# Performance work log

Measured on AMD Instinct MI355X. Metric: run time of the kernel, lower is better.

The kernel has to match this reference:

```python
import jax, jax.numpy as jnp
import numpy as np

B, S, E, HD = 8, 2048, 1024, 64  # batch, seq, n_embds, head_size (n_embds // n_heads)


def setup_inputs() -> dict:
    key = jax.random.key(0)
    k1, k2, k3, k4 = jax.random.split(key, 4)
    x = jax.random.normal(k1, (B, S, E), dtype=jnp.float32)
    # torch Linear weights have shape [out_features, in_features]; scale like default init
    Wk = jax.random.normal(k2, (HD, E), dtype=jnp.float32) * (1.0 / np.sqrt(E))
    Wq = jax.random.normal(k3, (HD, E), dtype=jnp.float32) * (1.0 / np.sqrt(E))
    Wv = jax.random.normal(k4, (HD, E), dtype=jnp.float32) * (1.0 / np.sqrt(E))
    return {"x": x, "Wk": Wk, "Wq": Wq, "Wv": Wv}


def reference(x, Wk, Wq, Wv):
    # q, k, v: [B, S, HD]
    k = jnp.einsum('bse,he->bsh', x, Wk)
    q = jnp.einsum('bse,he->bsh', x, Wq)
    v = jnp.einsum('bse,he->bsh', x, Wv)
    # scores: [B, S, S], scaled by sqrt(head_size)
    scores = jnp.einsum('bqh,bkh->bqk', q, k) / jnp.sqrt(jnp.float32(HD))
    # causal mask (tril): position q attends to k <= q
    causal = jnp.tril(jnp.ones((S, S), dtype=bool))
    scores = jnp.where(causal, scores, jnp.float32(-jnp.inf))
    attn = jax.nn.softmax(scores, axis=-1)
    # dropout_rate = 0.0 -> identity
    out = jnp.einsum('bqk,bkh->bqh', attn, v)  # [B, S, HD]
    return out
```

## Files before the change

### kernel.cpp

```cpp
#include <hip/hip_runtime.h>
#include <hip/hip_bf16.h>
#include <stdint.h>

typedef short bh8 __attribute__((ext_vector_type(8)));
typedef short bh4 __attribute__((ext_vector_type(4)));
typedef float fx4 __attribute__((ext_vector_type(4)));

#define B_ 8
#define S_ 2048
#define E_ 1024
#define HD_ 64

__device__ __forceinline__ short f2bf(float f) {
  unsigned u = __builtin_bit_cast(unsigned, f);
  u = u + 0x7FFFu + ((u >> 16) & 1u);
  return (short)(u >> 16);
}

#define GL2LDS16(gp, lp) __builtin_amdgcn_global_load_lds( \
    (const __attribute__((address_space(1))) unsigned int*)(gp), \
    (__attribute__((address_space(3))) unsigned int*)(lp), 16, 0, 0)


__global__ __launch_bounds__(256) void castw_k(
    const float* __restrict__ wk, const float* __restrict__ wq,
    const float* __restrict__ wv, short* __restrict__ wc) {
  int i = blockIdx.x * 256 + threadIdx.x;
  int wsel = i >> 13;
  int o = (i & 8191) * 8;
  const float* src = (wsel == 0) ? wk : (wsel == 1) ? wq : wv;
  float4 a = *(const float4*)(src + o);
  float4 b = *(const float4*)(src + o + 4);
  bh8 r = { f2bf(a.x), f2bf(a.y), f2bf(a.z), f2bf(a.w),
            f2bf(b.x), f2bf(b.y), f2bf(b.z), f2bf(b.w) };
  *(bh8*)(wc + wsel * (HD_ * E_) + o) = r;
}

__global__ __launch_bounds__(256) void qkv_gemm(
    const float* __restrict__ x, const short* __restrict__ wc,
    short* __restrict__ kfr, short* __restrict__ qfr, short* __restrict__ vfr) {
  __shared__ short As[2][32 * 32];
  __shared__ short Bs[2][192 * 32];
  const int tid = threadIdx.x;
  const int w = tid >> 6, l = tid & 63;
  const int c = l & 15, g = l >> 4;
  const int r0 = blockIdx.x * 32;
  const int srow = l >> 2;
  const int scol = (l & 3) * 8;
  const int ar = tid >> 3;
  const int ac = (tid & 7) * 4;
  const float* xrow = x + (size_t)(r0 + ar) * E_ + ac;

  fx4 acc[2][3];
#pragma unroll
  for (int rt = 0; rt < 2; ++rt)
#pragma unroll
    for (int cc = 0; cc < 3; ++cc) acc[rt][cc] = (fx4){0.f, 0.f, 0.f, 0.f};

  float4 av = *(const float4*)(xrow);
  {
    bh4 aw = { f2bf(av.x), f2bf(av.y), f2bf(av.z), f2bf(av.w) };
    *(bh4*)&As[0][ar * 32 + ac] = aw;
#pragma unroll
    for (int p = 0; p < 3; ++p)
      GL2LDS16(wc + (size_t)(16 * (w + 4 * p) + srow) * E_ + scol,
               &Bs[0][(w + 4 * p) * 512]);
    av = *(const float4*)(xrow + 32);
    __builtin_amdgcn_sched_barrier(0);
    asm volatile("s_waitcnt vmcnt(1) lgkmcnt(0)" ::: "memory");
    __builtin_amdgcn_s_barrier();
    __builtin_amdgcn_sched_barrier(0);
  }

  for (int t = 0; t < 32; ++t) {
    const int cur = t & 1;
    if (t < 31) {
      bh4 aw = { f2bf(av.x), f2bf(av.y), f2bf(av.z), f2bf(av.w) };
      *(bh4*)&As[cur ^ 1][ar * 32 + ac] = aw;
      const int k1 = (t + 1) * 32;
#pragma unroll
      for (int p = 0; p < 3; ++p)
        GL2LDS16(wc + (size_t)(16 * (w + 4 * p) + srow) * E_ + k1 + scol,
                 &Bs[cur ^ 1][(w + 4 * p) * 512]);
      const int k2 = (t + 2 < 32) ? (t + 2) * 32 : 0;
      av = *(const float4*)(xrow + k2);
      __builtin_amdgcn_sched_barrier(0);
    }

    bh8 af[2], bf[3];
    af[0] = *(const bh8*)&As[cur][c * 32 + 8 * g];
    af[1] = *(const bh8*)&As[cur][(16 + c) * 32 + 8 * g];
#pragma unroll
    for (int cc = 0; cc < 3; ++cc)
      bf[cc] = *(const bh8*)&Bs[cur][(16 * (3 * w + cc) + c) * 32 + 8 * g];
#pragma unroll
    for (int rt = 0; rt < 2; ++rt)
#pragma unroll
      for (int cc = 0; cc < 3; ++cc)
        acc[rt][cc] = __builtin_amdgcn_mfma_f32_16x16x32_bf16(af[rt], bf[cc], acc[rt][cc], 0, 0, 0);

    if (t < 31) {
      __builtin_amdgcn_sched_barrier(0);
      asm volatile("s_waitcnt vmcnt(1) lgkmcnt(0)" ::: "memory");
      __builtin_amdgcn_s_barrier();
      __builtin_amdgcn_sched_barrier(0);
    }
  }

#pragma unroll
  for (int rt = 0; rt < 2; ++rt) {
    const int rbase = r0 + 16 * rt + 4 * g;
    const int bb = rbase >> 11;
    const int srw = rbase & (S_ - 1);
    const int kt = srw >> 4;
    const int g2 = (srw & 15) >> 2;
#pragma unroll
    for (int cc = 0; cc < 3; ++cc) {
      const int ctg = 3 * w + cc;
      const int n = 16 * ctg + c;
      if (ctg < 4) {
        const int h = n >> 5, gg = (n & 31) >> 3, jj = n & 7;
        short* dst = kfr + ((size_t)(((bb * 128 + kt) * 2 + h) * 64 + gg * 16) * 8) + jj;
#pragma unroll
        for (int j = 0; j < 4; ++j)
          dst[(size_t)(((rbase + j) & 15)) * 8] = f2bf(acc[rt][cc][j]);
      } else if (ctg < 8) {
        const int nq = n - 64;
        const int h = nq >> 5, gg = (nq & 31) >> 3, jj = nq & 7;
        short* dst = qfr + ((size_t)(((bb * 128 + kt) * 2 + h) * 64 + gg * 16) * 8) + jj;
#pragma unroll
        for (int j = 0; j < 4; ++j)
          dst[(size_t)(((rbase + j) & 15)) * 8] = f2bf(acc[rt][cc][j] * 0.125f);
      } else {
        const int hd = n - 128;
        const int mm = hd >> 4, c2 = hd & 15;
        bh4 pk = { f2bf(acc[rt][cc][0]), f2bf(acc[rt][cc][1]),
                   f2bf(acc[rt][cc][2]), f2bf(acc[rt][cc][3]) };
        *(bh4*)&vfr[(size_t)(((bb * 128 + kt) * 4 + mm) * 64 + g2 * 16 + c2) * 4] = pk;
      }
    }
  }
}

__global__ __launch_bounds__(512, 4) void attn_fused3(
    const short* __restrict__ qfr, const short* __restrict__ kfr,
    const short* __restrict__ vfr, float* __restrict__ out) {
  __shared__ float sO[8][16][68];
  __shared__ float sL[8][16];
  const int tid = threadIdx.x;
  const int w = tid >> 6, l = tid & 63;
  const int c = l & 15, g = l >> 4;
  const int b = blockIdx.x >> 6, p = blockIdx.x & 63;
  const int qtA = p, qtB = 127 - p;

  const short* qbB = qfr + (size_t)(b * 128) * 1024;
  const short* kbB = kfr + (size_t)(b * 128) * 1024;
  const short* vbB = vfr + (size_t)(b * 128) * 1024;

  bh8 qA0 = *(const bh8*)(qbB + (qtA * 2 + 0) * 512 + l * 8);
  bh8 qA1 = *(const bh8*)(qbB + (qtA * 2 + 1) * 512 + l * 8);
  bh8 qB0 = *(const bh8*)(qbB + (qtB * 2 + 0) * 512 + l * 8);
  bh8 qB1 = *(const bh8*)(qbB + (qtB * 2 + 1) * 512 + l * 8);

  fx4 oA[4], oB[4];
#pragma unroll
  for (int mm = 0; mm < 4; ++mm) { oA[mm] = (fx4){0,0,0,0}; oB[mm] = (fx4){0,0,0,0}; }
  float lA = 0.f, lB = 0.f;

  for (int kt = w; kt <= qtB; kt += 8) {
    const short* kp = kbB + kt * 1024;
    bh8 kf0 = *(const bh8*)(kp + l * 8);
    bh8 kf1 = *(const bh8*)(kp + 512 + l * 8);
    const short* vp = vbB + kt * 1024;
    bh4 vf0 = *(const bh4*)(vp + l * 4);
    bh4 vf1 = *(const bh4*)(vp + 256 + l * 4);
    bh4 vf2 = *(const bh4*)(vp + 512 + l * 4);
    bh4 vf3 = *(const bh4*)(vp + 768 + l * 4);

    fx4 sB = {0.f, 0.f, 0.f, 0.f};
    sB = __builtin_amdgcn_mfma_f32_16x16x32_bf16(kf0, qB0, sB, 0, 0, 0);
    sB = __builtin_amdgcn_mfma_f32_16x16x32_bf16(kf1, qB1, sB, 0, 0, 0);
    if (kt == qtB) {
#pragma unroll
      for (int j = 0; j < 4; ++j)
        if (4 * g + j > c) sB[j] = -1e30f;
    }
    const float pB0 = __expf(sB[0] - 8.f);
    const float pB1 = __expf(sB[1] - 8.f);
    const float pB2 = __expf(sB[2] - 8.f);
    const float pB3 = __expf(sB[3] - 8.f);
    lB += (pB0 + pB1) + (pB2 + pB3);
    bh4 pfB = { f2bf(pB0), f2bf(pB1), f2bf(pB2), f2bf(pB3) };
    oB[0] = __builtin_amdgcn_mfma_f32_16x16x16bf16_1k(vf0, pfB, oB[0], 0, 0, 0);
    oB[1] = __builtin_amdgcn_mfma_f32_16x16x16bf16_1k(vf1, pfB, oB[1], 0, 0, 0);
    oB[2] = __builtin_amdgcn_mfma_f32_16x16x16bf16_1k(vf2, pfB, oB[2], 0, 0, 0);
    oB[3] = __builtin_amdgcn_mfma_f32_16x16x16bf16_1k(vf3, pfB, oB[3], 0, 0, 0);

    if (kt <= qtA) {
      fx4 sA = {0.f, 0.f, 0.f, 0.f};
      sA = __builtin_amdgcn_mfma_f32_16x16x32_bf16(kf0, qA0, sA, 0, 0, 0);
      sA = __builtin_amdgcn_mfma_f32_16x16x32_bf16(kf1, qA1, sA, 0, 0, 0);
      if (kt == qtA) {
#pragma unroll
        for (int j = 0; j < 4; ++j)
          if (4 * g + j > c) sA[j] = -1e30f;
      }
      const float pA0 = __expf(sA[0] - 8.f);
      const float pA1 = __expf(sA[1] - 8.f);
      const float pA2 = __expf(sA[2] - 8.f);
      const float pA3 = __expf(sA[3] - 8.f);
      lA += (pA0 + pA1) + (pA2 + pA3);
      bh4 pfA = { f2bf(pA0), f2bf(pA1), f2bf(pA2), f2bf(pA3) };
      oA[0] = __builtin_amdgcn_mfma_f32_16x16x16bf16_1k(vf0, pfA, oA[0], 0, 0, 0);
      oA[1] = __builtin_amdgcn_mfma_f32_16x16x16bf16_1k(vf1, pfA, oA[1], 0, 0, 0);
      oA[2] = __builtin_amdgcn_mfma_f32_16x16x16bf16_1k(vf2, pfA, oA[2], 0, 0, 0);
      oA[3] = __builtin_amdgcn_mfma_f32_16x16x16bf16_1k(vf3, pfA, oA[3], 0, 0, 0);
    }
  }

#pragma unroll
  for (int mm = 0; mm < 4; ++mm)
    *(fx4*)&sO[w][c][16 * mm + 4 * g] = oA[mm];
  lA += __shfl_xor(lA, 16, 64);
  lA += __shfl_xor(lA, 32, 64);
  if (g == 0) sL[w][c] = lA;
  __syncthreads();
  if (w < 4) {
    const int r = tid >> 4;
    const int cg4 = (tid & 15) * 4;
    fx4 a = {0.f, 0.f, 0.f, 0.f};
    float L = 0.f;
#pragma unroll
    for (int i = 0; i < 8; ++i) { a += *(const fx4*)&sO[i][r][cg4]; L += sL[i][r]; }
    fx4 res = a * (1.0f / L);
    *(fx4*)(out + ((size_t)(b * S_ + qtA * 16 + r)) * HD_ + cg4) = res;
  }
  __syncthreads();
#pragma unroll
  for (int mm = 0; mm < 4; ++mm)
    *(fx4*)&sO[w][c][16 * mm + 4 * g] = oB[mm];
  lB += __shfl_xor(lB, 16, 64);
  lB += __shfl_xor(lB, 32, 64);
  if (g == 0) sL[w][c] = lB;
  __syncthreads();
  if (w < 4) {
    const int r = tid >> 4;
    const int cg4 = (tid & 15) * 4;
    fx4 a = {0.f, 0.f, 0.f, 0.f};
    float L = 0.f;
#pragma unroll
    for (int i = 0; i < 8; ++i) { a += *(const fx4*)&sO[i][r][cg4]; L += sL[i][r]; }
    fx4 res = a * (1.0f / L);
    *(fx4*)(out + ((size_t)(b * S_ + qtB * 16 + r)) * HD_ + cg4) = res;
  }
}

extern "C" void kernel_launch(void* const* d_in, const int* in_sizes, int n_in,
                              void* d_out, int out_size, void* d_ws, size_t ws_size,
                              hipStream_t stream) {
  const float* x  = (const float*)d_in[0];
  const float* wk = (const float*)d_in[1];
  const float* wq = (const float*)d_in[2];
  const float* wv = (const float*)d_in[3];
  float* out = (float*)d_out;
  char* ws = (char*)d_ws;
  short* wc  = (short*)(ws);
  short* kfr = (short*)(ws + 393216);
  short* qfr = (short*)(ws + 2490368);
  short* vfr = (short*)(ws + 4587520);

  castw_k<<<dim3(96), dim3(256), 0, stream>>>(wk, wq, wv, wc);
  qkv_gemm<<<dim3(512), dim3(256), 0, stream>>>(x, wc, kfr, qfr, vfr);
  attn_fused3<<<dim3(512), dim3(512), 0, stream>>>(qfr, kfr, vfr, out);
}
```

Baseline: 49.67 us.

## Load x fragments directly into registers in QKV GEMM, dropping A LDS staging

The QKV projection GEMM no longer stages the fp32 input tile into shared memory as bf16. Each wave now loads its own 16-row slice of x straight from global memory in MFMA fragment layout, converts it in registers, and computes six output column tiles instead of a 2x3 grid. This removes the A-tile LDS writes and reads and their bank traffic. In exchange, each x element is loaded from global memory by two waves instead of once per block, and fewer B fragments are reused per A fragment.

```diff
diff --git a/kernel.cpp b/kernel.cpp
--- a/kernel.cpp
+++ b/kernel.cpp
@@ -39,105 +39,94 @@
 __global__ __launch_bounds__(256) void qkv_gemm(
     const float* __restrict__ x, const short* __restrict__ wc,
     short* __restrict__ kfr, short* __restrict__ qfr, short* __restrict__ vfr) {
-  __shared__ short As[2][32 * 32];
   __shared__ short Bs[2][192 * 32];
   const int tid = threadIdx.x;
   const int w = tid >> 6, l = tid & 63;
   const int c = l & 15, g = l >> 4;
   const int r0 = blockIdx.x * 32;
+  const int wr = w & 1;
+  const int wcg = w >> 1;
   const int srow = l >> 2;
   const int scol = (l & 3) * 8;
-  const int ar = tid >> 3;
-  const int ac = (tid & 7) * 4;
-  const float* xrow = x + (size_t)(r0 + ar) * E_ + ac;
-
-  fx4 acc[2][3];
-#pragma unroll
-  for (int rt = 0; rt < 2; ++rt)
-#pragma unroll
-    for (int cc = 0; cc < 3; ++cc) acc[rt][cc] = (fx4){0.f, 0.f, 0.f, 0.f};
-
-  float4 av = *(const float4*)(xrow);
+  const float* xrow = x + (size_t)(r0 + 16 * wr + c) * E_ + 8 * g;
+
+  fx4 acc[6];
+#pragma unroll
+  for (int cc = 0; cc < 6; ++cc) acc[cc] = (fx4){0.f, 0.f, 0.f, 0.f};
+
+  float4 xa0, xa1;
   {
-    bh4 aw = { f2bf(av.x), f2bf(av.y), f2bf(av.z), f2bf(av.w) };
-    *(bh4*)&As[0][ar * 32 + ac] = aw;
 #pragma unroll
     for (int p = 0; p < 3; ++p)
       GL2LDS16(wc + (size_t)(16 * (w + 4 * p) + srow) * E_ + scol,
                &Bs[0][(w + 4 * p) * 512]);
-    av = *(const float4*)(xrow + 32);
+    xa0 = *(const float4*)(xrow);
+    xa1 = *(const float4*)(xrow + 4);
     __builtin_amdgcn_sched_barrier(0);
-    asm volatile("s_waitcnt vmcnt(1) lgkmcnt(0)" ::: "memory");
+    asm volatile("s_waitcnt vmcnt(2)" ::: "memory");
     __builtin_amdgcn_s_barrier();
     __builtin_amdgcn_sched_barrier(0);
   }
 
   for (int t = 0; t < 32; ++t) {
     const int cur = t & 1;
+    float4 xb0, xb1;
     if (t < 31) {
-      bh4 aw = { f2bf(av.x), f2bf(av.y), f2bf(av.z), f2bf(av.w) };
-      *(bh4*)&As[cur ^ 1][ar * 32 + ac] = aw;
       const int k1 = (t + 1) * 32;
 #pragma unroll
       for (int p = 0; p < 3; ++p)
         GL2LDS16(wc + (size_t)(16 * (w + 4 * p) + srow) * E_ + k1 + scol,
                  &Bs[cur ^ 1][(w + 4 * p) * 512]);
-      const int k2 = (t + 2 < 32) ? (t + 2) * 32 : 0;
-      av = *(const float4*)(xrow + k2);
+      xb0 = *(const float4*)(xrow + k1);
+      xb1 = *(const float4*)(xrow + k1 + 4);
       __builtin_amdgcn_sched_barrier(0);
     }
 
-    bh8 af[2], bf[3];
-    af[0] = *(const bh8*)&As[cur][c * 32 + 8 * g];
-    af[1] = *(const bh8*)&As[cur][(16 + c) * 32 + 8 * g];
-#pragma unroll
-    for (int cc = 0; cc < 3; ++cc)
-      bf[cc] = *(const bh8*)&Bs[cur][(16 * (3 * w + cc) + c) * 32 + 8 * g];
-#pragma unroll
-    for (int rt = 0; rt < 2; ++rt)
-#pragma unroll
-      for (int cc = 0; cc < 3; ++cc)
-        acc[rt][cc] = __builtin_amdgcn_mfma_f32_16x16x32_bf16(af[rt], bf[cc], acc[rt][cc], 0, 0, 0);
+    bh8 af = { f2bf(xa0.x), f2bf(xa0.y), f2bf(xa0.z), f2bf(xa0.w),
+               f2bf(xa1.x), f2bf(xa1.y), f2bf(xa1.z), f2bf(xa1.w) };
+#pragma unroll
+    for (int cc = 0; cc < 6; ++cc) {
+      bh8 bf = *(const bh8*)&Bs[cur][(16 * (6 * wcg + cc) + c) * 32 + 8 * g];
+      acc[cc] = __builtin_amdgcn_mfma_f32_16x16x32_bf16(af, bf, acc[cc], 0, 0, 0);
+    }
 
     if (t < 31) {
+      xa0 = xb0; xa1 = xb1;
       __builtin_amdgcn_sched_barrier(0);
-      asm volatile("s_waitcnt vmcnt(1) lgkmcnt(0)" ::: "memory");
+      asm volatile("s_waitcnt vmcnt(2) lgkmcnt(0)" ::: "memory");
       __builtin_amdgcn_s_barrier();
       __builtin_amdgcn_sched_barrier(0);
     }
   }
 
-#pragma unroll
-  for (int rt = 0; rt < 2; ++rt) {
-    const int rbase = r0 + 16 * rt + 4 * g;
-    const int bb = rbase >> 11;
-    const int srw = rbase & (S_ - 1);
-    const int kt = srw >> 4;
-    const int g2 = (srw & 15) >> 2;
-#pragma unroll
-    for (int cc = 0; cc < 3; ++cc) {
-      const int ctg = 3 * w + cc;
-      const int n = 16 * ctg + c;
-      if (ctg < 4) {
-        const int h = n >> 5, gg = (n & 31) >> 3, jj = n & 7;
-        short* dst = kfr + ((size_t)(((bb * 128 + kt) * 2 + h) * 64 + gg * 16) * 8) + jj;
-#pragma unroll
-        for (int j = 0; j < 4; ++j)
-          dst[(size_t)(((rbase + j) & 15)) * 8] = f2bf(acc[rt][cc][j]);
-      } else if (ctg < 8) {
-        const int nq = n - 64;
-        const int h = nq >> 5, gg = (nq & 31) >> 3, jj = nq & 7;
-        short* dst = qfr + ((size_t)(((bb * 128 + kt) * 2 + h) * 64 + gg * 16) * 8) + jj;
-#pragma unroll
-        for (int j = 0; j < 4; ++j)
-          dst[(size_t)(((rbase + j) & 15)) * 8] = f2bf(acc[rt][cc][j] * 0.125f);
-      } else {
-        const int hd = n - 128;
-        const int mm = hd >> 4, c2 = hd & 15;
-        bh4 pk = { f2bf(acc[rt][cc][0]), f2bf(acc[rt][cc][1]),
-                   f2bf(acc[rt][cc][2]), f2bf(acc[rt][cc][3]) };
-        *(bh4*)&vfr[(size_t)(((bb * 128 + kt) * 4 + mm) * 64 + g2 * 16 + c2) * 4] = pk;
-      }
+  const int rbase = r0 + 16 * wr + 4 * g;
+  const int bb = rbase >> 11;
+  const int srw = rbase & (S_ - 1);
+  const int kt = srw >> 4;
+  const int g2 = (srw & 15) >> 2;
+#pragma unroll
+  for (int cc = 0; cc < 6; ++cc) {
+    const int ctg = 6 * wcg + cc;
+    const int n = 16 * ctg + c;
+    if (ctg < 4) {
+      const int h = n >> 5, gg = (n & 31) >> 3, jj = n & 7;
+      short* dst = kfr + ((size_t)(((bb * 128 + kt) * 2 + h) * 64 + gg * 16) * 8) + jj;
+#pragma unroll
+      for (int j = 0; j < 4; ++j)
+        dst[(size_t)(((rbase + j) & 15)) * 8] = f2bf(acc[cc][j]);
+    } else if (ctg < 8) {
+      const int nq = n - 64;
+      const int h = nq >> 5, gg = (nq & 31) >> 3, jj = nq & 7;
+      short* dst = qfr + ((size_t)(((bb * 128 + kt) * 2 + h) * 64 + gg * 16) * 8) + jj;
+#pragma unroll
+      for (int j = 0; j < 4; ++j)
+        dst[(size_t)(((rbase + j) & 15)) * 8] = f2bf(acc[cc][j] * 0.125f);
+    } else {
+      const int hd = n - 128;
+      const int mm = hd >> 4, c2 = hd & 15;
+      bh4 pk = { f2bf(acc[cc][0]), f2bf(acc[cc][1]),
+                 f2bf(acc[cc][2]), f2bf(acc[cc][3]) };
+      *(bh4*)&vfr[(size_t)(((bb * 128 + kt) * 4 + mm) * 64 + g2 * 16 + c2) * 4] = pk;
     }
   }
 }
```

New measurement: 55.89 us. +12.5%, slower.
